# Performance work log

Hardware: AMD Instinct MI355X
Metric: run time of the kernel (lower is better)

Reference implementation:

```python
import jax, jax.numpy as jnp
import numpy as np

N = 100000      # nodes
E = 800000      # edges
F_IN = 128      # input feature dim
HID = 8         # per-head hidden
HEADS = 8
HD = HID * HEADS  # 64
G = 128         # graphs in batch
C = 10          # classes
SLOPE = 0.2     # leaky relu negative slope


def setup_inputs() -> dict:
    key = jax.random.key(0)
    ks = iter(jax.random.split(key, 48))
    def rn(shape, scale=0.1):
        return jax.random.normal(next(ks), shape, jnp.float32) * scale
    inp = {
        'x': jax.random.normal(next(ks), (N, F_IN), jnp.float32),
        'edge_index': jax.random.randint(next(ks), (2, E), 0, N),
        'batch': jnp.sort(jax.random.randint(next(ks), (N,), 0, G)),
        # GAT layer 1
        'W1': rn((F_IN, HEADS * HID)), 'as1': rn((HEADS, HID)), 'ad1': rn((HEADS, HID)), 'b1': jnp.zeros((HEADS * HID,), jnp.float32),
        # GAT layer 2
        'W2': rn((HD, HEADS * HID)), 'as2': rn((HEADS, HID)), 'ad2': rn((HEADS, HID)), 'b2': jnp.zeros((HEADS * HID,), jnp.float32),
        # node attention MLP (HD -> HD//2 -> 2)
        'na_w1': rn((HD, HD // 2)), 'na_b1': jnp.zeros((HD // 2,), jnp.float32), 'na_w2': rn((HD // 2, 2)), 'na_b2': jnp.zeros((2,), jnp.float32),
        # edge attention MLP (2*HD -> HD -> 2)
        'ea_w1': rn((2 * HD, HD)), 'ea_b1': jnp.zeros((HD,), jnp.float32), 'ea_w2': rn((HD, 2)), 'ea_b2': jnp.zeros((2,), jnp.float32),
        # GCN causal / trivial
        'gc_w': rn((HD, HD)), 'gc_b': jnp.zeros((HD,), jnp.float32),
        'gt_w': rn((HD, HD)), 'gt_b': jnp.zeros((HD,), jnp.float32),
        # readouts
        'rc_w': rn((HD, HD)), 'rc_b': jnp.zeros((HD,), jnp.float32),
        'rt_w': rn((HD, HD)), 'rt_b': jnp.zeros((HD,), jnp.float32),
        # classifiers (HD -> HD//2 -> C), combined (2HD -> HD -> C)
        'cc_w1': rn((HD, HD // 2)), 'cc_b1': jnp.zeros((HD // 2,), jnp.float32), 'cc_w2': rn((HD // 2, C)), 'cc_b2': jnp.zeros((C,), jnp.float32),
        'ct_w1': rn((HD, HD // 2)), 'ct_b1': jnp.zeros((HD // 2,), jnp.float32), 'ct_w2': rn((HD // 2, C)), 'ct_b2': jnp.zeros((C,), jnp.float32),
        'cm_w1': rn((2 * HD, HD)), 'cm_b1': jnp.zeros((HD,), jnp.float32), 'cm_w2': rn((HD, C)), 'cm_b2': jnp.zeros((C,), jnp.float32),
    }
    return inp


def _mlp2(h, w1, b1, w2, b2):
    return jax.nn.relu(h @ w1 + b1) @ w2 + b2


def reference(x, edge_index, batch,
              W1, as1, ad1, b1, W2, as2, ad2, b2,
              na_w1, na_b1, na_w2, na_b2,
              ea_w1, ea_b1, ea_w2, ea_b2,
              gc_w, gc_b, gt_w, gt_b,
              rc_w, rc_b, rt_w, rt_b,
              cc_w1, cc_b1, cc_w2, cc_b2,
              ct_w1, ct_b1, ct_w2, ct_b2,
              cm_w1, cm_b1, cm_w2, cm_b2):
    src, dst = edge_index[0], edge_index[1]
    loop = jnp.arange(N)
    s2 = jnp.concatenate([src, loop])  # edges + self-loops (PyG GATConv/GCNConv add self-loops)
    d2 = jnp.concatenate([dst, loop])

    def gat(h_in, W, a_s, a_d, b):
        h = (h_in @ W).reshape(N, HEADS, HID)
        es = jnp.einsum('nhd,hd->nh', h, a_s)
        ed = jnp.einsum('nhd,hd->nh', h, a_d)
        logit = jax.nn.leaky_relu(es[s2] + ed[d2], SLOPE)      # [E+N, H]
        m = jax.ops.segment_max(logit, d2, num_segments=N)
        ex = jnp.exp(logit - m[d2])
        den = jax.ops.segment_sum(ex, d2, num_segments=N)
        alpha = ex / (den[d2] + 1e-16)
        out = jax.ops.segment_sum(h[s2] * alpha[..., None], d2, num_segments=N)
        return out.reshape(N, HEADS * HID) + b

    # GNN encoder (dropout disabled: eval mode)
    H1 = jax.nn.elu(gat(x, W1, as1, ad1, b1))
    H = gat(H1, W2, as2, ad2, b2)                              # [N, HD]

    # node attention
    na = jax.nn.softmax(_mlp2(H, na_w1, na_b1, na_w2, na_b2), axis=1)
    alpha_c, alpha_t = na[:, 0], na[:, 1]
    # edge attention (original edges, no self-loops)
    ef = jnp.concatenate([H[src], H[dst]], axis=1)             # [E, 2*HD]
    ea = jax.nn.softmax(_mlp2(ef, ea_w1, ea_b1, ea_w2, ea_b2), axis=1)
    beta_c, beta_t = ea[:, 0], ea[:, 1]

    Hc = H * alpha_c[:, None]
    Ht = H * alpha_t[:, None]

    def gcn(h_in, w, b, ew):
        # PyG gcn_norm: self-loops with weight 1, symmetric deg^-1/2 normalization
        w_full = jnp.concatenate([ew, jnp.ones((N,), h_in.dtype)])
        deg = jax.ops.segment_sum(w_full, d2, num_segments=N)
        dis = jnp.where(deg > 0, jax.lax.rsqrt(jnp.maximum(deg, 1e-20)), 0.0)
        norm = dis[s2] * w_full * dis[d2]
        h = h_in @ w
        return jax.ops.segment_sum(h[s2] * norm[:, None], d2, num_segments=N) + b

    Gc = gcn(Hc, gc_w, gc_b, beta_c)
    Gt = gcn(Ht, gt_w, gt_b, beta_t)

    # readout: linear then global_add_pool
    hGc = jax.ops.segment_sum(Gc @ rc_w + rc_b, batch, num_segments=G)  # [G, HD]
    hGt = jax.ops.segment_sum(Gt @ rt_w + rt_b, batch, num_segments=G)

    zc = _mlp2(hGc, cc_w1, cc_b1, cc_w2, cc_b2)
    zt = _mlp2(hGt, ct_w1, ct_b1, ct_w2, ct_b2)
    # RandomIntervention: within-graph node shuffle followed by add-pool == plain add-pool
    h_comb = jnp.concatenate([hGc + hGt], axis=1) if False else (hGc + hGt)
    zp = _mlp2(jnp.concatenate([h_comb, jnp.zeros_like(h_comb)], axis=1), cm_w1, cm_b1, cm_w2, cm_b2) if False else _mlp2_comb(h_comb, cm_w1, cm_b1, cm_w2, cm_b2)
    return (zc, zt, zp, hGc, hGt)


def _mlp2_comb(h_comb, cm_w1, cm_b1, cm_w2, cm_b2):
    # original: classifier_combined takes hidden_dim*2 input; forward feeds h_G_c + shuffled_h_G_t
    # which is [G, HD]; to match Linear(2*HD, ...) we use the first HD rows of cm_w1 twice?
    # NO -- the original code as written passes a [G, HD] tensor to a Linear(2*HD, HD) layer,
    # which would error in torch. Faithful runnable interpretation: combined feature is
    # concat([h_G_c, shuffled_h_G_t]) of width 2*HD (the standard CAL formulation).
    return jax.nn.relu(h_comb @ cm_w1 + cm_b1) @ cm_w2 + cm_b2


# clean final definition overriding the commented exploration above
def reference(x, edge_index, batch,
              W1, as1, ad1, b1, W2, as2, ad2, b2,
              na_w1, na_b1, na_w2, na_b2,
              ea_w1, ea_b1, ea_w2, ea_b2,
              gc_w, gc_b, gt_w, gt_b,
              rc_w, rc_b, rt_w, rt_b,
              cc_w1, cc_b1, cc_w2, cc_b2,
              ct_w1, ct_b1, ct_w2, ct_b2,
              cm_w1, cm_b1, cm_w2, cm_b2):
    src, dst = edge_index[0], edge_index[1]
    loop = jnp.arange(N)
    s2 = jnp.concatenate([src, loop])
    d2 = jnp.concatenate([dst, loop])

    def gat(h_in, W, a_s, a_d, b):
        h = (h_in @ W).reshape(N, HEADS, HID)
        es = jnp.einsum('nhd,hd->nh', h, a_s)
        ed = jnp.einsum('nhd,hd->nh', h, a_d)
        logit = jax.nn.leaky_relu(es[s2] + ed[d2], SLOPE)
        m = jax.ops.segment_max(logit, d2, num_segments=N)
        ex = jnp.exp(logit - m[d2])
        den = jax.ops.segment_sum(ex, d2, num_segments=N)
        alpha = ex / (den[d2] + 1e-16)
        out = jax.ops.segment_sum(h[s2] * alpha[..., None], d2, num_segments=N)
        return out.reshape(N, HEADS * HID) + b

    H1 = jax.nn.elu(gat(x, W1, as1, ad1, b1))
    H = gat(H1, W2, as2, ad2, b2)

    na = jax.nn.softmax(_mlp2(H, na_w1, na_b1, na_w2, na_b2), axis=1)
    alpha_c, alpha_t = na[:, 0], na[:, 1]
    ef = jnp.concatenate([H[src], H[dst]], axis=1)
    ea = jax.nn.softmax(_mlp2(ef, ea_w1, ea_b1, ea_w2, ea_b2), axis=1)
    beta_c, beta_t = ea[:, 0], ea[:, 1]

    Hc = H * alpha_c[:, None]
    Ht = H * alpha_t[:, None]

    def gcn(h_in, w, b, ew):
        w_full = jnp.concatenate([ew, jnp.ones((N,), h_in.dtype)])
        deg = jax.ops.segment_sum(w_full, d2, num_segments=N)
        dis = jnp.where(deg > 0, jax.lax.rsqrt(jnp.maximum(deg, 1e-20)), 0.0)
        norm = dis[s2] * w_full * dis[d2]
        h = h_in @ w
        return jax.ops.segment_sum(h[s2] * norm[:, None], d2, num_segments=N) + b

    Gc = gcn(Hc, gc_w, gc_b, beta_c)
    Gt = gcn(Ht, gt_w, gt_b, beta_t)

    hGc = jax.ops.segment_sum(Gc @ rc_w + rc_b, batch, num_segments=G)
    hGt = jax.ops.segment_sum(Gt @ rt_w + rt_b, batch, num_segments=G)

    zc = _mlp2(hGc, cc_w1, cc_b1, cc_w2, cc_b2)
    zt = _mlp2(hGt, ct_w1, ct_b1, ct_w2, ct_b2)
    # RandomIntervention with sorted batch: within-graph permutation + add-pool == add-pool
    h_comb = jnp.concatenate([hGc, hGt], axis=1)  # [G, 2*HD] for Linear(2*HD, ...)
    zp = _mlp2(h_comb, cm_w1, cm_b1, cm_w2, cm_b2)
    return (zc, zt, zp, hGc, hGt)


if __name__ == '__main__':
    out = reference(**setup_inputs())
    print([o.shape for o in out])
```

## Files before the change

kernel.cpp:

```cpp
#include <hip/hip_runtime.h>
#include <hip/hip_bf16.h>

#define N_NODES 100000
#define E_EDGES 800000
#define E2 (E_EDGES + N_NODES)
#define FIN 128
#define HD 64
#define NH 8
#define NG 128
#define NC 10
#define SLOPE 0.2f
#define SELF_FLAG 0x40000000
#define SRC_MASK  0x3FFFFFFF
#define NSCAN_BLK 391
#define NBLK64 1563
#define GB 16
#define ECAP 256
#define NPW 8
#define EA_BLKS 3125
#define AG_BLKS 6250

#define U1_STRIPES 261
#define U1_GRID (2 + U1_STRIPES * 7)
#define U1_HISTB (U1_STRIPES * 4)
#define T1 (U1_STRIPES * 3)
#define U2_STRIPES 391
#define U2_GRID (U2_STRIPES * 11)

typedef unsigned short bfu;

__device__ __forceinline__ float lrelu(float x) { return x > 0.f ? x : SLOPE * x; }

__device__ __forceinline__ bfu f2bf(float f) {
    unsigned int u = __float_as_uint(f);
    u += 0x7FFFu + ((u >> 16) & 1u);
    return (bfu)(u >> 16);
}
__device__ __forceinline__ float bf2f(bfu s) {
    return __uint_as_float(((unsigned int)s) << 16);
}
__device__ __forceinline__ float bflo(unsigned int u) { return __uint_as_float(u << 16); }
__device__ __forceinline__ float bfhi(unsigned int u) { return __uint_as_float(u & 0xFFFF0000u); }

template<typename TIN, int KIN, int MODE>
__device__ __forceinline__
void gemm_tile_body(float* smem, int tile,
                    const TIN* __restrict__ in, const float* __restrict__ W,
                    bfu* __restrict__ outB,
                    const float* __restrict__ a_s, const float* __restrict__ a_d,
                    float* __restrict__ es, float* __restrict__ ed)
{
    constexpr int KH = (KIN > 64) ? 64 : KIN;
    constexpr int RS = KIN + 4;
    float* Ws   = smem;
    float* rows = smem + KH * 64;
    int t = threadIdx.x;
    int base = tile * 64;

    if constexpr (sizeof(TIN) == 4) {
        constexpr int RQ = KIN / 4;
        for (int i = t; i < 64 * RQ; i += 256) {
            int r = i / RQ, c = (i % RQ) * 4;
            int n = base + r;
            float4 v = make_float4(0.f, 0.f, 0.f, 0.f);
            if (n < N_NODES) v = *(const float4*)((const float*)in + (size_t)n * KIN + c);
            *(float4*)(rows + r * RS + c) = v;
        }
    } else {
        constexpr int RQ = KIN / 8;
        for (int i = t; i < 64 * RQ; i += 256) {
            int r = i / RQ, c = (i % RQ) * 8;
            int n = base + r;
            uint4 v = make_uint4(0, 0, 0, 0);
            if (n < N_NODES) v = *(const uint4*)((const bfu*)in + (size_t)n * KIN + c);
            float* dp = rows + r * RS + c;
            *(float4*)dp       = make_float4(bflo(v.x), bfhi(v.x), bflo(v.y), bfhi(v.y));
            *(float4*)(dp + 4) = make_float4(bflo(v.z), bfhi(v.z), bflo(v.w), bfhi(v.w));
        }
    }

    int tr = t >> 4, tc = t & 15;
    float acc[4][4] = {};
    const float4* R4 = (const float4*)rows;

    for (int h = 0; h < KIN / KH; ++h) {
        __syncthreads();
        {
            const float4* Wv = (const float4*)(W + (size_t)h * KH * 64);
            float4* Wsv4 = (float4*)Ws;
            for (int i = t; i < KH * 16; i += 256) Wsv4[i] = Wv[i];
        }
        __syncthreads();
        const float4* Wsv = (const float4*)Ws;
#pragma unroll 2
        for (int k = 0; k < KH; k += 4) {
            float4 w0 = Wsv[(k + 0) * 16 + tc];
            float4 w1 = Wsv[(k + 1) * 16 + tc];
            float4 w2 = Wsv[(k + 2) * 16 + tc];
            float4 w3 = Wsv[(k + 3) * 16 + tc];
            int kq = (h * KH + k) >> 2;
#pragma unroll
            for (int i = 0; i < 4; ++i) {
                float4 r = R4[(tr * 4 + i) * (RS / 4) + kq];
                acc[i][0] = fmaf(r.x, w0.x, fmaf(r.y, w1.x, fmaf(r.z, w2.x, fmaf(r.w, w3.x, acc[i][0]))));
                acc[i][1] = fmaf(r.x, w0.y, fmaf(r.y, w1.y, fmaf(r.z, w2.y, fmaf(r.w, w3.y, acc[i][1]))));
                acc[i][2] = fmaf(r.x, w0.z, fmaf(r.y, w1.z, fmaf(r.z, w2.z, fmaf(r.w, w3.z, acc[i][2]))));
                acc[i][3] = fmaf(r.x, w0.w, fmaf(r.y, w1.w, fmaf(r.z, w2.w, fmaf(r.w, w3.w, acc[i][3]))));
            }
        }
    }

    int j0 = tc * 4;
#pragma unroll
    for (int i = 0; i < 4; ++i) {
        int n = base + tr * 4 + i;
        if (n < N_NODES) {
            ushort4 ov;
            ov.x = f2bf(acc[i][0]); ov.y = f2bf(acc[i][1]);
            ov.z = f2bf(acc[i][2]); ov.w = f2bf(acc[i][3]);
            *(ushort4*)(outB + (size_t)n * 64 + j0) = ov;
        }
    }
    if (MODE == 1) {
        float s0[4], s1[4];
#pragma unroll
        for (int i = 0; i < 4; ++i) {
            float pes = 0.f, ped = 0.f;
#pragma unroll
            for (int q = 0; q < 4; ++q) {
                pes = fmaf(acc[i][q], a_s[j0 + q], pes);
                ped = fmaf(acc[i][q], a_d[j0 + q], ped);
            }
            pes += __shfl_xor(pes, 1, 64);
            ped += __shfl_xor(ped, 1, 64);
            s0[i] = pes; s1[i] = ped;
        }
        if ((tc & 1) == 0) {
            int h = tc >> 1;
#pragma unroll
            for (int i = 0; i < 4; ++i) {
                int n = base + tr * 4 + i;
                if (n < N_NODES) {
                    es[n * NH + h] = s0[i];
                    ed[n * NH + h] = s1[i];
                }
            }
        }
    }
}

__device__ __forceinline__
void weight_prep_body(float* smem,
                      const float* __restrict__ gw, const float* __restrict__ gb,
                      const float* __restrict__ rw, const float* __restrict__ rb,
                      float* __restrict__ Wp, float* __restrict__ bp)
{
    float* A = smem;
    float* B = smem + 4096;
    int t = threadIdx.x;
    {
        const float4* ga = (const float4*)gw;
        const float4* rA = (const float4*)rw;
        float4* dA = (float4*)A; float4* dB = (float4*)B;
        for (int i = t; i < 1024; i += 256) { dA[i] = ga[i]; dB[i] = rA[i]; }
    }
    __syncthreads();
    for (int e = t * 16; e < t * 16 + 16; ++e) {
        int k = e >> 6, j = e & 63;
        float acc = 0.f;
#pragma unroll 8
        for (int m = 0; m < 64; ++m) acc = fmaf(A[k * 64 + m], B[m * 64 + j], acc);
        Wp[e] = acc;
    }
    if (t < 64) {
        float acc = rb[t];
#pragma unroll 8
        for (int m = 0; m < 64; ++m) acc = fmaf(gb[m], B[m * 64 + t], acc);
        bp[t] = acc;
    }
}

__global__ __launch_bounds__(256)
void u1_fused(const float* __restrict__ x, const float* __restrict__ W1,
              bfu* __restrict__ B0, const float* __restrict__ as1,
              const float* __restrict__ ad1, float* __restrict__ es,
              float* __restrict__ ed,
              const int* __restrict__ ei, int* __restrict__ cnt,
              int* __restrict__ rank,
              const float* __restrict__ gc_w, const float* __restrict__ gc_b,
              const float* __restrict__ rc_w, const float* __restrict__ rc_b,
              const float* __restrict__ gt_w, const float* __restrict__ gt_b,
              const float* __restrict__ rt_w, const float* __restrict__ rt_b,
              float* __restrict__ Wcp, float* __restrict__ bcp,
              float* __restrict__ Wtp, float* __restrict__ btp)
{
    __shared__ __align__(16) float smem[12544];
    int b = blockIdx.x;
    if (b < 2) {
        if (b == 0) weight_prep_body(smem, gc_w, gc_b, rc_w, rc_b, Wcp, bcp);
        else        weight_prep_body(smem, gt_w, gt_b, rt_w, rt_b, Wtp, btp);
        return;
    }
    int u = b - 2;
    int stripe = u / 7, r = u % 7;
    if (r < 3) {
        gemm_tile_body<float, FIN, 1>(smem, stripe * 3 + r, x, W1, B0, as1, ad1, es, ed);
    } else {
        int idx = stripe * 4 + (r - 3);
        int t = threadIdx.x;
        const int STR = U1_HISTB * 256;
        for (int e = idx * 256 + t; e < E_EDGES; e += 2 * STR) {
            int e1 = e + STR;
            int d0 = ei[E_EDGES + e];
            int r0 = atomicAdd(&cnt[d0], 1);
            int r1 = 0;
            bool has1 = e1 < E_EDGES;
            if (has1) r1 = atomicAdd(&cnt[ei[E_EDGES + e1]], 1);
            rank[e] = r0;
            if (has1) rank[e1] = r1;
        }
    }
}

__global__ __launch_bounds__(256)
void u2_fused(const float* __restrict__ x, const float* __restrict__ W1,
              bfu* __restrict__ B0, const float* __restrict__ as1,
              const float* __restrict__ ad1, float* __restrict__ es,
              float* __restrict__ ed,
              const int* __restrict__ ei, const int* __restrict__ rank,
              const int* __restrict__ offs,
              int* __restrict__ csr)
{
    __shared__ __align__(16) float smem[12544];
    int b = blockIdx.x;
    int stripe = b / 11, r = b % 11;
    int t = threadIdx.x;
    if (r < 8) {
        int e = (stripe * 8 + r) * 256 + t;
        if (e < E_EDGES) {
            int s = ei[e], d = ei[E_EDGES + e];
            csr[offs[d] + rank[e]] = s;
        }
    } else if (r < 10) {
        int tile = T1 + stripe * 2 + (r - 8);
        if (tile < NBLK64)
            gemm_tile_body<float, FIN, 1>(smem, tile, x, W1, B0, as1, ad1, es, ed);
    } else {
        int n = stripe * 256 + t;
        if (n < N_NODES) {
            csr[offs[n + 1] - 1] = n | SELF_FLAG;
        }
    }
}

__global__ __launch_bounds__(256)
void u3_fused(const bfu* __restrict__ in,
              const float* __restrict__ na_w1, const float* __restrict__ na_b1,
              const float* __restrict__ na_w2, const float* __restrict__ na_b2,
              float2* __restrict__ al2,
              const float* __restrict__ ea_w1,
              bfu* __restrict__ out0, bfu* __restrict__ out1)
{
    __shared__ __align__(16) float smem[12544];
    float* Ws   = smem;
    float* rows = smem + 8192;
    int t = threadIdx.x;
    int base = blockIdx.x * 64;
    const float* W0 = ea_w1;
    const float* W1 = ea_w1 + 64 * 64;
    {
        const float4* W0v = (const float4*)W0;
        const float4* W1v = (const float4*)W1;
        float4* Wsv = (float4*)Ws;
        for (int i = t; i < 1024; i += 256) { Wsv[i] = W0v[i]; Wsv[1024 + i] = W1v[i]; }
    }
    for (int i = t; i < 64 * 8; i += 256) {
        int r = i >> 3, c = (i & 7) * 8;
        int n = base + r;
        uint4 v = make_uint4(0, 0, 0, 0);
        if (n < N_NODES) v = *(const uint4*)(in + (size_t)n * 64 + c);
        float* dp = rows + r * 68 + c;
        *(float4*)dp       = make_float4(bflo(v.x), bfhi(v.x), bflo(v.y), bfhi(v.y));
        *(float4*)(dp + 4) = make_float4(bflo(v.z), bfhi(v.z), bflo(v.w), bfhi(v.w));
    }
    __syncthreads();
    {
        int tr = t >> 4, tc = t & 15;
        float a0[4][4] = {}, a1[4][4] = {};
        const float4* Wsv = (const float4*)Ws;
        const float4* R4 = (const float4*)rows;
#pragma unroll 2
        for (int k = 0; k < 64; k += 4) {
            float4 p0 = Wsv[(k + 0) * 16 + tc];
            float4 p1 = Wsv[(k + 1) * 16 + tc];
            float4 p2 = Wsv[(k + 2) * 16 + tc];
            float4 p3 = Wsv[(k + 3) * 16 + tc];
            float4 q0 = Wsv[1024 + (k + 0) * 16 + tc];
            float4 q1 = Wsv[1024 + (k + 1) * 16 + tc];
            float4 q2 = Wsv[1024 + (k + 2) * 16 + tc];
            float4 q3 = Wsv[1024 + (k + 3) * 16 + tc];
            int kq = k >> 2;
#pragma unroll
            for (int i = 0; i < 4; ++i) {
                float4 r = R4[(tr * 4 + i) * 17 + kq];
                a0[i][0] = fmaf(r.x, p0.x, fmaf(r.y, p1.x, fmaf(r.z, p2.x, fmaf(r.w, p3.x, a0[i][0]))));
                a0[i][1] = fmaf(r.x, p0.y, fmaf(r.y, p1.y, fmaf(r.z, p2.y, fmaf(r.w, p3.y, a0[i][1]))));
                a0[i][2] = fmaf(r.x, p0.z, fmaf(r.y, p1.z, fmaf(r.z, p2.z, fmaf(r.w, p3.z, a0[i][2]))));
                a0[i][3] = fmaf(r.x, p0.w, fmaf(r.y, p1.w, fmaf(r.z, p2.w, fmaf(r.w, p3.w, a0[i][3]))));
                a1[i][0] = fmaf(r.x, q0.x, fmaf(r.y, q1.x, fmaf(r.z, q2.x, fmaf(r.w, q3.x, a1[i][0]))));
                a1[i][1] = fmaf(r.x, q0.y, fmaf(r.y, q1.y, fmaf(r.z, q2.y, fmaf(r.w, q3.y, a1[i][1]))));
                a1[i][2] = fmaf(r.x, q0.z, fmaf(r.y, q1.z, fmaf(r.z, q2.z, fmaf(r.w, q3.z, a1[i][2]))));
                a1[i][3] = fmaf(r.x, q0.w, fmaf(r.y, q1.w, fmaf(r.z, q2.w, fmaf(r.w, q3.w, a1[i][3]))));
            }
        }
        int j0 = tc * 4;
#pragma unroll
        for (int i = 0; i < 4; ++i) {
            int n = base + tr * 4 + i;
            if (n >= N_NODES) continue;
            ushort4 o0, o1;
            o0.x = f2bf(a0[i][0]); o0.y = f2bf(a0[i][1]);
            o0.z = f2bf(a0[i][2]); o0.w = f2bf(a0[i][3]);
            o1.x = f2bf(a1[i][0]); o1.y = f2bf(a1[i][1]);
            o1.z = f2bf(a1[i][2]); o1.w = f2bf(a1[i][3]);
            *(ushort4*)(out0 + (size_t)n * 64 + j0) = o0;
            *(ushort4*)(out1 + (size_t)n * 64 + j0) = o1;
        }
    }
    __syncthreads();
    {
        const float4* w1v = (const float4*)na_w1;
        float4* dst = (float4*)Ws;
        for (int i = t; i < 512; i += 256) dst[i] = w1v[i];
        if (t < 64) Ws[2048 + t] = na_w2[t];
    }
    __syncthreads();
    {
        int tr = t >> 3;
        int tc = t & 7;
        float4 bv = *(const float4*)(na_b1 + tc * 4);
        float4 acc0 = bv, acc1 = bv;
        const float4* w1sv = (const float4*)Ws;
#pragma unroll 8
        for (int k = 0; k < 64; ++k) {
            float4 w = w1sv[k * 8 + tc];
            float r0 = rows[tr * 68 + k];
            float r1 = rows[(tr + 32) * 68 + k];
            acc0.x = fmaf(r0, w.x, acc0.x); acc0.y = fmaf(r0, w.y, acc0.y);
            acc0.z = fmaf(r0, w.z, acc0.z); acc0.w = fmaf(r0, w.w, acc0.w);
            acc1.x = fmaf(r1, w.x, acc1.x); acc1.y = fmaf(r1, w.y, acc1.y);
            acc1.z = fmaf(r1, w.z, acc1.z); acc1.w = fmaf(r1, w.w, acc1.w);
        }
        float z00 = 0.f, z01 = 0.f, z10 = 0.f, z11 = 0.f;
        float h0, w20, w21;
        int j0 = tc * 4;
#pragma unroll
        for (int q = 0; q < 4; ++q) {
            float a0q = q == 0 ? acc0.x : q == 1 ? acc0.y : q == 2 ? acc0.z : acc0.w;
            float a1q = q == 0 ? acc1.x : q == 1 ? acc1.y : q == 2 ? acc1.z : acc1.w;
            w20 = Ws[2048 + (j0 + q) * 2]; w21 = Ws[2048 + (j0 + q) * 2 + 1];
            h0 = fmaxf(a0q, 0.f);
            z00 = fmaf(h0, w20, z00); z01 = fmaf(h0, w21, z01);
            h0 = fmaxf(a1q, 0.f);
            z10 = fmaf(h0, w20, z10); z11 = fmaf(h0, w21, z11);
        }
#pragma unroll
        for (int o = 1; o < 8; o <<= 1) {
            z00 += __shfl_xor(z00, o, 64); z01 += __shfl_xor(z01, o, 64);
            z10 += __shfl_xor(z10, o, 64); z11 += __shfl_xor(z11, o, 64);
        }
        if (tc == 0) {
            int n0 = base + tr, n1 = base + tr + 32;
            if (n0 < N_NODES) {
                float zz0 = z00 + na_b2[0], zz1 = z01 + na_b2[1];
                float mx = fmaxf(zz0, zz1);
                float e0 = __expf(zz0 - mx), e1 = __expf(zz1 - mx);
                float ss = e0 + e1;
                al2[n0] = make_float2(e0 / ss, e1 / ss);
            }
            if (n1 < N_NODES) {
                float zz0 = z10 + na_b2[0], zz1 = z11 + na_b2[1];
                float mx = fmaxf(zz0, zz1);
                float e0 = __expf(zz0 - mx), e1 = __expf(zz1 - mx);
                float ss = e0 + e1;
                al2[n1] = make_float2(e0 / ss, e1 / ss);
            }
        }
    }
}

__global__ __launch_bounds__(256)
void gemm_tile_k64(const bfu* __restrict__ in, const float* __restrict__ W,
                   bfu* __restrict__ outB,
                   const float* __restrict__ a_s, const float* __restrict__ a_d,
                   float* __restrict__ es, float* __restrict__ ed)
{
    __shared__ __align__(16) float smem[64 * 64 + 64 * 68];
    gemm_tile_body<bfu, 64, 1>(smem, blockIdx.x, in, W, outB, a_s, a_d, es, ed);
}

__global__ void csr_scan1(const int* __restrict__ cnt, int* __restrict__ offs,
                          int* __restrict__ bsum, const int* __restrict__ batch,
                          int* __restrict__ glo)
{
    __shared__ int tmp[256];
    int t = threadIdx.x;
    int i = blockIdx.x * 256 + t;
    int v = (i < N_NODES) ? cnt[i] + 1 : 0;
    tmp[t] = v; __syncthreads();
#pragma unroll
    for (int o = 1; o < 256; o <<= 1) {
        int a = (t >= o) ? tmp[t - o] : 0;
        __syncthreads();
        tmp[t] += a;
        __syncthreads();
    }
    if (i < N_NODES) offs[i] = tmp[t] - v;
    if (t == 255) bsum[blockIdx.x] = tmp[255];
    if (blockIdx.x == 0 && t <= NG) {
        int l = 0, r = N_NODES;
        while (l < r) { int m = (l + r) >> 1; if (batch[m] < t) l = m + 1; else r = m; }
        glo[t] = l;
    }
}

__global__ void csr_scan23(int* __restrict__ offs, const int* __restrict__ bsum)
{
    __shared__ int tmp[256];
    int b = blockIdx.x;
    int t = threadIdx.x;
    int s = 0;
    for (int j = t; j < b; j += 256) s += bsum[j];
    tmp[t] = s; __syncthreads();
#pragma unroll
    for (int o = 128; o > 0; o >>= 1) {
        if (t < o) tmp[t] += tmp[t + o];
        __syncthreads();
    }
    int prefix = tmp[0];
    int i = b * 256 + t;
    if (i < N_NODES) offs[i] += prefix;
    if (i == 0) offs[N_NODES] = E2;
}

template<int ELU>
__global__ void gat_aggregate4(const int* __restrict__ offs, const int* __restrict__ csr,
                               const float* __restrict__ es, const float* __restrict__ ed,
                               const bfu* __restrict__ hsrcB, const float* __restrict__ bias,
                               bfu* __restrict__ outB)
{
    int w = threadIdx.x >> 6;
    int lane = threadIdx.x & 63;
    int slot = lane >> 4;
    int fl = lane & 15;
    int h  = fl >> 1;
    int n = (blockIdx.x * 4 + w) * 4 + slot;
    if (n >= N_NODES) return;
    float4 bv = *(const float4*)(bias + fl * 4);
    int beg = offs[n], end = offs[n + 1];
    float edv = ed[n * NH + h];
    float den = 0.f;
    float4 acc = make_float4(0.f, 0.f, 0.f, 0.f);
    int p = beg;
    for (; p + 1 < end; p += 2) {
        int s0 = csr[p] & SRC_MASK;
        int s1 = csr[p + 1] & SRC_MASK;
        float ex0 = __expf(lrelu(es[s0 * NH + h] + edv));
        float ex1 = __expf(lrelu(es[s1 * NH + h] + edv));
        den += ex0 + ex1;
        ushort4 ra = *(const ushort4*)(hsrcB + (size_t)s0 * HD + fl * 4);
        ushort4 rb = *(const ushort4*)(hsrcB + (size_t)s1 * HD + fl * 4);
        acc.x = fmaf(bf2f(ra.x), ex0, fmaf(bf2f(rb.x), ex1, acc.x));
        acc.y = fmaf(bf2f(ra.y), ex0, fmaf(bf2f(rb.y), ex1, acc.y));
        acc.z = fmaf(bf2f(ra.z), ex0, fmaf(bf2f(rb.z), ex1, acc.z));
        acc.w = fmaf(bf2f(ra.w), ex0, fmaf(bf2f(rb.w), ex1, acc.w));
    }
    if (p < end) {
        int s = csr[p] & SRC_MASK;
        float ex = __expf(lrelu(es[s * NH + h] + edv));
        den += ex;
        ushort4 rb = *(const ushort4*)(hsrcB + (size_t)s * HD + fl * 4);
        acc.x = fmaf(bf2f(rb.x), ex, acc.x);
        acc.y = fmaf(bf2f(rb.y), ex, acc.y);
        acc.z = fmaf(bf2f(rb.z), ex, acc.z);
        acc.w = fmaf(bf2f(rb.w), ex, acc.w);
    }
    float inv = 1.f / (den + 1e-16f);
    float v0 = acc.x * inv + bv.x;
    float v1 = acc.y * inv + bv.y;
    float v2 = acc.z * inv + bv.z;
    float v3 = acc.w * inv + bv.w;
    if (ELU) {
        v0 = v0 > 0.f ? v0 : (__expf(v0) - 1.f);
        v1 = v1 > 0.f ? v1 : (__expf(v1) - 1.f);
        v2 = v2 > 0.f ? v2 : (__expf(v2) - 1.f);
        v3 = v3 > 0.f ? v3 : (__expf(v3) - 1.f);
    }
    ushort4 ov;
    ov.x = f2bf(v0); ov.y = f2bf(v1); ov.z = f2bf(v2); ov.w = f2bf(v3);
    *(ushort4*)(outB + (size_t)n * HD + fl * 4) = ov;
}

__global__ __launch_bounds__(256)
void edge_att_node(const int* __restrict__ offs, const int* __restrict__ csr,
                   const bfu* __restrict__ P1b, const bfu* __restrict__ P2b,
                   const float* __restrict__ b1, const float* __restrict__ w2,
                   const float* __restrict__ b2,
                   const float2* __restrict__ al2,
                   float2* __restrict__ beta2,
                   float2* __restrict__ prod2)
{
    __shared__ float2 bbuf[4][ECAP];
    int w = threadIdx.x >> 6;
    int lane = threadIdx.x & 63;
    int nbase = (blockIdx.x * 4 + w) * NPW;
    if (nbase >= N_NODES) return;
    int slot = lane >> 3, q = lane & 7;
    const float4* pb = (const float4*)(b1 + q * 8);
    const float4* pw = (const float4*)(w2 + q * 16);
    float4 c0 = pb[0], c1 = pb[1];
    float4 w0 = pw[0], w1v = pw[1], w2v = pw[2], w3v = pw[3];
    float wd0 = w0.x - w0.y,   wd1 = w0.z - w0.w;
    float wd2 = w1v.x - w1v.y, wd3 = w1v.z - w1v.w;
    float wd4 = w2v.x - w2v.y, wd5 = w2v.z - w2v.w;
    float wd6 = w3v.x - w3v.y, wd7 = w3v.z - w3v.w;
    float zbd = b2[0] - b2[1];
    for (int j = 0; j < NPW; ++j) {
        int n = nbase + j;
        if (n >= N_NODES) return;
        uint4 U2 = *(const uint4*)(P2b + (size_t)n * 64 + q * 8);
        float d0 = bflo(U2.x) + c0.x, d1 = bfhi(U2.x) + c0.y;
        float d2 = bflo(U2.y) + c0.z, d3 = bfhi(U2.y) + c0.w;
        float d4 = bflo(U2.z) + c1.x, d5 = bfhi(U2.z) + c1.y;
        float d6 = bflo(U2.w) + c1.z, d7 = bfhi(U2.w) + c1.w;
        int beg = offs[n], endr = offs[n + 1] - 1;
        int m = endr - beg;
        float dc = 0.f, dt = 0.f;
        for (int p = beg + slot; p < endr; p += 8) {
            int s = csr[p];
            uint4 U1 = *(const uint4*)(P1b + (size_t)s * 64 + q * 8);
            float h0 = fmaxf(bflo(U1.x) + d0, 0.f);
            float h1 = fmaxf(bfhi(U1.x) + d1, 0.f);
            float h2 = fmaxf(bflo(U1.y) + d2, 0.f);
            float h3 = fmaxf(bfhi(U1.y) + d3, 0.f);
            float h4 = fmaxf(bflo(U1.z) + d4, 0.f);
            float h5 = fmaxf(bfhi(U1.z) + d5, 0.f);
            float h6 = fmaxf(bflo(U1.w) + d6, 0.f);
            float h7 = fmaxf(bfhi(U1.w) + d7, 0.f);
            float z = fmaf(h0, wd0, fmaf(h1, wd1, fmaf(h2, wd2, fmaf(h3, wd3,
                      fmaf(h4, wd4, fmaf(h5, wd5, fmaf(h6, wd6, h7 * wd7)))))));
            z += __shfl_xor(z, 1, 64);
            z += __shfl_xor(z, 2, 64);
            z += __shfl_xor(z, 4, 64);
            if (q == 0) {
                z += zbd;
                float e = __expf(-fabsf(z));
                float inv = 1.f / (1.f + e);
                float bx = z >= 0.f ? inv : e * inv;
                float by = z >= 0.f ? e * inv : inv;
                int idx = p - beg;
                if (idx < ECAP) bbuf[w][idx] = make_float2(bx, by);
                else            beta2[p]    = make_float2(bx, by);
                dc += bx; dt += by;
            }
        }
        dc += __shfl_xor(dc, 8, 64);  dt += __shfl_xor(dt, 8, 64);
        dc += __shfl_xor(dc, 16, 64); dt += __shfl_xor(dt, 16, 64);
        dc += __shfl_xor(dc, 32, 64); dt += __shfl_xor(dt, 32, 64);
        dc = __shfl(dc, 0, 64); dt = __shfl(dt, 0, 64);
        dc += 1.f; dt += 1.f;
        float ic = rsqrtf(fmaxf(dc, 1e-20f));
        float it = rsqrtf(fmaxf(dt, 1e-20f));
        if (lane == 0) {
            float2 al = al2[n];
            prod2[n] = make_float2(ic * al.x, it * al.y);
        }
        if (m > ECAP)
            asm volatile("s_waitcnt vmcnt(0)" ::: "memory");
        for (int idx = lane; idx <= m; idx += 64) {
            float2 v = (idx == m) ? make_float2(1.f, 1.f)
                     : (idx < ECAP) ? bbuf[w][idx] : beta2[beg + idx];
            beta2[beg + idx] = make_float2(v.x * ic, v.y * it);
        }
    }
}

__global__ __launch_bounds__(256)
void gcn_readout_fused(const int* __restrict__ offs, const int* __restrict__ csr,
                       const int* __restrict__ glo,
                       const bfu* __restrict__ HB,
                       const float2* __restrict__ beta2,
                       const float2* __restrict__ prod2,
                       float* __restrict__ Pc, float* __restrict__ Pt)
{
    int g = blockIdx.x / GB, b = blockIdx.x % GB;
    int t = threadIdx.x;
    int pbeg = offs[glo[g]], pend = offs[glo[g + 1]];
    int total = pend - pbeg;
    int chunk = (total + GB - 1) / GB;
    int start = pbeg + b * chunk;
    int end = start + chunk;
    if (end > pend) end = pend;
    if (start > pend) start = pend;
    int slot = t >> 4, fl = t & 15;
    float4 a1 = make_float4(0.f, 0.f, 0.f, 0.f);
    float4 a2 = make_float4(0.f, 0.f, 0.f, 0.f);
    int p = start + slot;
    for (; p + 48 < end; p += 64) {
#pragma unroll
        for (int j = 0; j < 4; ++j) {
            int pp = p + j * 16;
            int s = csr[pp] & SRC_MASK;
            float2 bb = beta2[pp];
            float2 pr = prod2[s];
            float wc = pr.x * bb.x;
            float wt = pr.y * bb.y;
            ushort4 r0 = *(const ushort4*)(HB + (size_t)s * HD + fl * 4);
            float f0 = bf2f(r0.x), f1 = bf2f(r0.y), f2 = bf2f(r0.z), f3 = bf2f(r0.w);
            a1.x = fmaf(f0, wc, a1.x); a1.y = fmaf(f1, wc, a1.y);
            a1.z = fmaf(f2, wc, a1.z); a1.w = fmaf(f3, wc, a1.w);
            a2.x = fmaf(f0, wt, a2.x); a2.y = fmaf(f1, wt, a2.y);
            a2.z = fmaf(f2, wt, a2.z); a2.w = fmaf(f3, wt, a2.w);
        }
    }
    for (; p < end; p += 16) {
        int s = csr[p] & SRC_MASK;
        float2 bb = beta2[p];
        float2 pr = prod2[s];
        float wc = pr.x * bb.x;
        float wt = pr.y * bb.y;
        ushort4 r0 = *(const ushort4*)(HB + (size_t)s * HD + fl * 4);
        float f0 = bf2f(r0.x), f1 = bf2f(r0.y), f2 = bf2f(r0.z), f3 = bf2f(r0.w);
        a1.x = fmaf(f0, wc, a1.x); a1.y = fmaf(f1, wc, a1.y);
        a1.z = fmaf(f2, wc, a1.z); a1.w = fmaf(f3, wc, a1.w);
        a2.x = fmaf(f0, wt, a2.x); a2.y = fmaf(f1, wt, a2.y);
        a2.z = fmaf(f2, wt, a2.z); a2.w = fmaf(f3, wt, a2.w);
    }
    __shared__ float redc[16 * 64], redt[16 * 64];
    *(float4*)(redc + slot * 64 + fl * 4) = a1;
    *(float4*)(redt + slot * 64 + fl * 4) = a2;
    __syncthreads();
    if (t < 64) {
        float sc = 0.f, st = 0.f;
#pragma unroll
        for (int s = 0; s < 16; ++s) { sc += redc[s * 64 + t]; st += redt[s * 64 + t]; }
        Pc[(size_t)blockIdx.x * 64 + t] = sc;
        Pt[(size_t)blockIdx.x * 64 + t] = st;
    }
}

__global__ __launch_bounds__(64)
void head_final(const float* __restrict__ Pc, const float* __restrict__ Pt,
                const int* __restrict__ glo,
                const float* __restrict__ Wcp, const float* __restrict__ bcp,
                const float* __restrict__ Wtp, const float* __restrict__ btp,
                const float* __restrict__ cc_w1, const float* __restrict__ cc_b1,
                const float* __restrict__ cc_w2, const float* __restrict__ cc_b2,
                const float* __restrict__ ct_w1, const float* __restrict__ ct_b1,
                const float* __restrict__ ct_w2, const float* __restrict__ ct_b2,
                const float* __restrict__ cm_w1, const float* __restrict__ cm_b1,
                const float* __restrict__ cm_w2, const float* __restrict__ cm_b2,
                float* __restrict__ out)
{
    int g = blockIdx.x;
    int t = threadIdx.x;
    __shared__ float scl[64], stl[64], hgc[64], hgt[64], hid[64];
    float sc = 0.f, st = 0.f;
#pragma unroll
    for (int b = 0; b < GB; ++b) {
        sc += Pc[(size_t)(g * GB + b) * 64 + t];
        st += Pt[(size_t)(g * GB + b) * 64 + t];
    }
    scl[t] = sc; stl[t] = st;
    float c = (float)(glo[g + 1] - glo[g]);
    __syncthreads();
    {
        float a = c * bcp[t], bb = c * btp[t];
#pragma unroll 8
        for (int k = 0; k < 64; ++k) {
            a  = fmaf(scl[k], Wcp[k * 64 + t], a);
            bb = fmaf(stl[k], Wtp[k * 64 + t], bb);
        }
        hgc[t] = a; hgt[t] = bb;
        out[3840 + g * 64 + t]  = a;
        out[12032 + g * 64 + t] = bb;
    }
    __syncthreads();
    if (t < 32) {
        float a = cc_b1[t];
#pragma unroll 8
        for (int k = 0; k < 64; ++k) a = fmaf(hgc[k], cc_w1[k * 32 + t], a);
        hid[t] = fmaxf(a, 0.f);
    }
    __syncthreads();
    if (t < NC) {
        float a = cc_b2[t];
#pragma unroll
        for (int k = 0; k < 32; ++k) a = fmaf(hid[k], cc_w2[k * NC + t], a);
        out[g * NC + t] = a;
    }
    __syncthreads();
    if (t < 32) {
        float a = ct_b1[t];
#pragma unroll 8
        for (int k = 0; k < 64; ++k) a = fmaf(hgt[k], ct_w1[k * 32 + t], a);
        hid[t] = fmaxf(a, 0.f);
    }
    __syncthreads();
    if (t < NC) {
        float a = ct_b2[t];
#pragma unroll
        for (int k = 0; k < 32; ++k) a = fmaf(hid[k], ct_w2[k * NC + t], a);
        out[1280 + g * NC + t] = a;
    }
    __syncthreads();
    {
        float a = cm_b1[t];
#pragma unroll 8
        for (int k = 0; k < 64; ++k) {
            a = fmaf(hgc[k], cm_w1[k * 64 + t], a);
            a = fmaf(hgt[k], cm_w1[(64 + k) * 64 + t], a);
        }
        hid[t] = fmaxf(a, 0.f);
    }
    __syncthreads();
    if (t < NC) {
        float a = cm_b2[t];
#pragma unroll 8
        for (int k = 0; k < 64; ++k) a = fmaf(hid[k], cm_w2[k * NC + t], a);
        out[2560 + g * NC + t] = a;
    }
}

extern "C" void kernel_launch(void* const* d_in, const int* in_sizes, int n_in,
                              void* d_out, int out_size, void* d_ws, size_t ws_size,
                              hipStream_t stream)
{
    const float* x     = (const float*)d_in[0];
    const int*   ei    = (const int*)d_in[1];
    const int*   batch = (const int*)d_in[2];
    const float* W1    = (const float*)d_in[3];
    const float* as1   = (const float*)d_in[4];
    const float* ad1   = (const float*)d_in[5];
    const float* b1    = (const float*)d_in[6];
    const float* W2    = (const float*)d_in[7];
    const float* as2   = (const float*)d_in[8];
    const float* ad2   = (const float*)d_in[9];
    const float* b2    = (const float*)d_in[10];
    const float* na_w1 = (const float*)d_in[11];
    const float* na_b1 = (const float*)d_in[12];
    const float* na_w2 = (const float*)d_in[13];
    const float* na_b2 = (const float*)d_in[14];
    const float* ea_w1 = (const float*)d_in[15];
    const float* ea_b1 = (const float*)d_in[16];
    const float* ea_w2 = (const float*)d_in[17];
    const float* ea_b2 = (const float*)d_in[18];
    const float* gc_w  = (const float*)d_in[19];
    const float* gc_b  = (const float*)d_in[20];
    const float* gt_w  = (const float*)d_in[21];
    const float* gt_b  = (const float*)d_in[22];
    const float* rc_w  = (const float*)d_in[23];
    const float* rc_b  = (const float*)d_in[24];
    const float* rt_w  = (const float*)d_in[25];
    const float* rt_b  = (const float*)d_in[26];
    const float* cc_w1 = (const float*)d_in[27];
    const float* cc_b1 = (const float*)d_in[28];
    const float* cc_w2 = (const float*)d_in[29];
    const float* cc_b2 = (const float*)d_in[30];
    const float* ct_w1 = (const float*)d_in[31];
    const float* ct_b1 = (const float*)d_in[32];
    const float* ct_w2 = (const float*)d_in[33];
    const float* ct_b2 = (const float*)d_in[34];
    const float* cm_w1 = (const float*)d_in[35];
    const float* cm_b1 = (const float*)d_in[36];
    const float* cm_w2 = (const float*)d_in[37];
    const float* cm_b2 = (const float*)d_in[38];
    float* out = (float*)d_out;

    float* ws = (float*)d_ws;
    size_t o = 0;
    const size_t nf = (size_t)N_NODES * HD;
    float* es    = ws + o; o += (size_t)N_NODES * NH;
    float* ed    = ws + o; o += (size_t)N_NODES * NH;
    float2* al2  = (float2*)(ws + o); o += (size_t)N_NODES * 2;
    float2* beta2= (float2*)(ws + o); o += (size_t)E2 * 2;
    float2* prod2= (float2*)(ws + o); o += (size_t)N_NODES * 2;
    bfu* B0      = (bfu*)(ws + o); o += nf / 2;
    bfu* B1      = (bfu*)(ws + o); o += nf / 2;
    bfu* B2      = (bfu*)(ws + o); o += nf / 2;
    bfu* BH1     = (bfu*)(ws + o); o += nf / 2;
    int* csr     = (int*)(ws + o); o += E2;
    int* offs    = (int*)(ws + o); o += N_NODES + 1;
    float* Pc    = ws + o; o += (size_t)NG * GB * 64;
    float* Pt    = ws + o; o += (size_t)NG * GB * 64;
    float* Wcp   = ws + o; o += 4096;
    float* Wtp   = ws + o; o += 4096;
    float* bcp   = ws + o; o += 64;
    float* btp   = ws + o; o += 64;
    int* glo     = (int*)(ws + o); o += NG + 2;
    int* cnt  = (int*)beta2;
    int* bsum = (int*)prod2;
    int* rank = (int*)B1;

    hipMemsetAsync(cnt, 0, (size_t)N_NODES * 4, stream);
    u1_fused<<<U1_GRID, 256, 0, stream>>>(x, W1, B0, as1, ad1, es, ed,
                                          ei, cnt, rank,
                                          gc_w, gc_b, rc_w, rc_b,
                                          gt_w, gt_b, rt_w, rt_b,
                                          Wcp, bcp, Wtp, btp);
    csr_scan1<<<NSCAN_BLK, 256, 0, stream>>>(cnt, offs, bsum, batch, glo);
    csr_scan23<<<NSCAN_BLK, 256, 0, stream>>>(offs, bsum);

    u2_fused<<<U2_GRID, 256, 0, stream>>>(x, W1, B0, as1, ad1, es, ed,
                                          ei, rank, offs, csr);

    gat_aggregate4<1><<<AG_BLKS, 256, 0, stream>>>(offs, csr, es, ed, B0, b1, BH1);

    gemm_tile_k64<<<NBLK64, 256, 0, stream>>>(BH1, W2, B0, as2, ad2, es, ed);
    gat_aggregate4<0><<<AG_BLKS, 256, 0, stream>>>(offs, csr, es, ed, B0, b2, B2);

    u3_fused<<<NBLK64, 256, 0, stream>>>(B2, na_w1, na_b1, na_w2, na_b2, al2,
                                         ea_w1, B0, B1);

    edge_att_node<<<EA_BLKS, 256, 0, stream>>>(offs, csr, B0, B1,
                                               ea_b1, ea_w2, ea_b2, al2,
                                               beta2, prod2);

    gcn_readout_fused<<<NG * GB, 256, 0, stream>>>(offs, csr, glo, B2,
                                                   beta2, prod2, Pc, Pt);

    head_final<<<NG, 64, 0, stream>>>(Pc, Pt, glo,
                                      Wcp, bcp, Wtp, btp,
                                      cc_w1, cc_b1, cc_w2, cc_b2,
                                      ct_w1, ct_b1, ct_w2, ct_b2,
                                      cm_w1, cm_b1, cm_w2, cm_b2, out);
    (void)in_sizes; (void)n_in; (void)out_size; (void)ws_size;
}
```

Measured before the change: 442.9 us.

## Fuse head MLP into GCN readout via last-block ticket, widen readout split

The separate head_final launch is removed. Each readout block now takes a per-graph atomic ticket, and the last block to finish a graph reduces the partials and runs the classifier MLPs. The ticket counters are reset in csr_scan1. The readout split per graph grows from 16 to 24 blocks, and the edge-count histogram loop becomes a fixed three-edge unrolled body. This saves one kernel launch and its tail, at the cost of threadfence and atomic ordering overhead and a longer tail on the last block of each graph.

```diff
diff --git a/kernel.cpp b/kernel.cpp
--- a/kernel.cpp
+++ b/kernel.cpp
@@ -14,7 +14,7 @@
 #define SRC_MASK  0x3FFFFFFF
 #define NSCAN_BLK 391
 #define NBLK64 1563
-#define GB 16
+#define GB 24
 #define ECAP 256
 #define NPW 8
 #define EA_BLKS 3125
@@ -209,16 +209,18 @@
         int idx = stripe * 4 + (r - 3);
         int t = threadIdx.x;
         const int STR = U1_HISTB * 256;
-        for (int e = idx * 256 + t; e < E_EDGES; e += 2 * STR) {
-            int e1 = e + STR;
-            int d0 = ei[E_EDGES + e];
-            int r0 = atomicAdd(&cnt[d0], 1);
-            int r1 = 0;
-            bool has1 = e1 < E_EDGES;
-            if (has1) r1 = atomicAdd(&cnt[ei[E_EDGES + e1]], 1);
-            rank[e] = r0;
-            if (has1) rank[e1] = r1;
-        }
+        int e0 = idx * 256 + t;
+        int e1 = e0 + STR;
+        int e2 = e0 + 2 * STR;
+        bool h1 = e1 < E_EDGES, h2 = e2 < E_EDGES;
+        int d0 = ei[E_EDGES + e0];
+        int r0 = atomicAdd(&cnt[d0], 1);
+        int r1 = 0, r2 = 0;
+        if (h1) r1 = atomicAdd(&cnt[ei[E_EDGES + e1]], 1);
+        if (h2) r2 = atomicAdd(&cnt[ei[E_EDGES + e2]], 1);
+        rank[e0] = r0;
+        if (h1) rank[e1] = r1;
+        if (h2) rank[e2] = r2;
     }
 }
 
@@ -401,7 +403,7 @@
 
 __global__ void csr_scan1(const int* __restrict__ cnt, int* __restrict__ offs,
                           int* __restrict__ bsum, const int* __restrict__ batch,
-                          int* __restrict__ glo)
+                          int* __restrict__ glo, int* __restrict__ tickets)
 {
     __shared__ int tmp[256];
     int t = threadIdx.x;
@@ -422,6 +424,7 @@
         while (l < r) { int m = (l + r) >> 1; if (batch[m] < t) l = m + 1; else r = m; }
         glo[t] = l;
     }
+    if (blockIdx.x == 0 && t < NG) tickets[t] = 0;
 }
 
 __global__ void csr_scan23(int* __restrict__ offs, const int* __restrict__ bsum)
@@ -591,7 +594,17 @@
                        const bfu* __restrict__ HB,
                        const float2* __restrict__ beta2,
                        const float2* __restrict__ prod2,
-                       float* __restrict__ Pc, float* __restrict__ Pt)
+                       float* __restrict__ Pc, float* __restrict__ Pt,
+                       int* __restrict__ tickets,
+                       const float* __restrict__ Wcp, const float* __restrict__ bcp,
+                       const float* __restrict__ Wtp, const float* __restrict__ btp,
+                       const float* __restrict__ cc_w1, const float* __restrict__ cc_b1,
+                       const float* __restrict__ cc_w2, const float* __restrict__ cc_b2,
+                       const float* __restrict__ ct_w1, const float* __restrict__ ct_b1,
+                       const float* __restrict__ ct_w2, const float* __restrict__ ct_b2,
+                       const float* __restrict__ cm_w1, const float* __restrict__ cm_b1,
+                       const float* __restrict__ cm_w2, const float* __restrict__ cm_b2,
+                       float* __restrict__ out)
 {
     int g = blockIdx.x / GB, b = blockIdx.x % GB;
     int t = threadIdx.x;
@@ -637,6 +650,7 @@
         a2.z = fmaf(f2, wt, a2.z); a2.w = fmaf(f3, wt, a2.w);
     }
     __shared__ float redc[16 * 64], redt[16 * 64];
+    __shared__ int sflag;
     *(float4*)(redc + slot * 64 + fl * 4) = a1;
     *(float4*)(redt + slot * 64 + fl * 4) = a2;
     __syncthreads();
@@ -647,34 +661,32 @@
         Pc[(size_t)blockIdx.x * 64 + t] = sc;
         Pt[(size_t)blockIdx.x * 64 + t] = st;
     }
-}
-
-__global__ __launch_bounds__(64)
-void head_final(const float* __restrict__ Pc, const float* __restrict__ Pt,
-                const int* __restrict__ glo,
-                const float* __restrict__ Wcp, const float* __restrict__ bcp,
-                const float* __restrict__ Wtp, const float* __restrict__ btp,
-                const float* __restrict__ cc_w1, const float* __restrict__ cc_b1,
-                const float* __restrict__ cc_w2, const float* __restrict__ cc_b2,
-                const float* __restrict__ ct_w1, const float* __restrict__ ct_b1,
-                const float* __restrict__ ct_w2, const float* __restrict__ ct_b2,
-                const float* __restrict__ cm_w1, const float* __restrict__ cm_b1,
-                const float* __restrict__ cm_w2, const float* __restrict__ cm_b2,
-                float* __restrict__ out)
-{
-    int g = blockIdx.x;
-    int t = threadIdx.x;
-    __shared__ float scl[64], stl[64], hgc[64], hgt[64], hid[64];
-    float sc = 0.f, st = 0.f;
-#pragma unroll
-    for (int b = 0; b < GB; ++b) {
-        sc += Pc[(size_t)(g * GB + b) * 64 + t];
-        st += Pt[(size_t)(g * GB + b) * 64 + t];
-    }
-    scl[t] = sc; stl[t] = st;
+    __threadfence();
+    __syncthreads();
+    if (t == 0) {
+        int old = atomicAdd(&tickets[g], 1);
+        sflag = (old == GB - 1);
+    }
+    __syncthreads();
+    if (!sflag) return;
+    __threadfence();
+    float* scl = redc;
+    float* stl = redc + 64;
+    float* hgc = redc + 128;
+    float* hgt = redc + 192;
+    float* hid = redc + 256;
     float c = (float)(glo[g + 1] - glo[g]);
-    __syncthreads();
-    {
+    if (t < 64) {
+        float sc = 0.f, st = 0.f;
+#pragma unroll 8
+        for (int bb = 0; bb < GB; ++bb) {
+            sc += Pc[(size_t)(g * GB + bb) * 64 + t];
+            st += Pt[(size_t)(g * GB + bb) * 64 + t];
+        }
+        scl[t] = sc; stl[t] = st;
+    }
+    __syncthreads();
+    if (t < 64) {
         float a = c * bcp[t], bb = c * btp[t];
 #pragma unroll 8
         for (int k = 0; k < 64; ++k) {
@@ -714,7 +726,7 @@
         out[1280 + g * NC + t] = a;
     }
     __syncthreads();
-    {
+    if (t < 64) {
         float a = cm_b1[t];
 #pragma unroll 8
         for (int k = 0; k < 64; ++k) {
@@ -798,6 +810,7 @@
     float* bcp   = ws + o; o += 64;
     float* btp   = ws + o; o += 64;
     int* glo     = (int*)(ws + o); o += NG + 2;
+    int* tickets = (int*)(ws + o); o += NG;
     int* cnt  = (int*)beta2;
     int* bsum = (int*)prod2;
     int* rank = (int*)B1;
@@ -808,7 +821,7 @@
                                           gc_w, gc_b, rc_w, rc_b,
                                           gt_w, gt_b, rt_w, rt_b,
                                           Wcp, bcp, Wtp, btp);
-    csr_scan1<<<NSCAN_BLK, 256, 0, stream>>>(cnt, offs, bsum, batch, glo);
+    csr_scan1<<<NSCAN_BLK, 256, 0, stream>>>(cnt, offs, bsum, batch, glo, tickets);
     csr_scan23<<<NSCAN_BLK, 256, 0, stream>>>(offs, bsum);
 
     u2_fused<<<U2_GRID, 256, 0, stream>>>(x, W1, B0, as1, ad1, es, ed,
@@ -827,12 +840,10 @@
                                                beta2, prod2);
 
     gcn_readout_fused<<<NG * GB, 256, 0, stream>>>(offs, csr, glo, B2,
-                                                   beta2, prod2, Pc, Pt);
-
-    head_final<<<NG, 64, 0, stream>>>(Pc, Pt, glo,
-                                      Wcp, bcp, Wtp, btp,
-                                      cc_w1, cc_b1, cc_w2, cc_b2,
-                                      ct_w1, ct_b1, ct_w2, ct_b2,
-                                      cm_w1, cm_b1, cm_w2, cm_b2, out);
+                                                   beta2, prod2, Pc, Pt, tickets,
+                                                   Wcp, bcp, Wtp, btp,
+                                                   cc_w1, cc_b1, cc_w2, cc_b2,
+                                                   ct_w1, ct_b1, ct_w2, ct_b2,
+                                                   cm_w1, cm_b1, cm_w2, cm_b2, out);
     (void)in_sizes; (void)n_in; (void)out_size; (void)ws_size;
 }
```

After: 796.3 us. +79.8%, slower.
